# Kernel optimization log

Hardware: AMD Instinct MI355X
Metric: run time of the kernel (lower is better)

Reference implementation:

```python
import jax, jax.numpy as jnp
import numpy as np

T, B, D_POSE, H, K_CODES = 30, 1024, 135, 512, 512
EPS = 1e-5


def _bn_relu(x, g, b):
    # BatchNorm1d (training-mode batch stats, biased var) + ReLU; x: (B, C, L)
    m = x.mean(axis=(0, 2), keepdims=True)
    v = x.var(axis=(0, 2), keepdims=True)
    y = g[None, :, None] * (x - m) * jax.lax.rsqrt(v + EPS) + b[None, :, None]
    return jax.nn.relu(y)


def _conv_sk(x, w):
    # Conv1d with stride == kernel_size (non-overlapping): pure reshaped GEMM.
    # x: (B, I, L), w: (O, I, K) torch layout -> (B, O, L//K)
    Bn, I, L = x.shape
    O, _, K = w.shape
    xr = x.reshape(Bn, I, L // K, K)
    return jnp.einsum('bitk,oik->bot', xr, w)


def _convT_sk(x, w):
    # ConvTranspose1d with stride == kernel_size: x (B, I, L), w (I, O, K) torch layout
    Bn, I, L = x.shape
    _, O, K = w.shape
    return jnp.einsum('bil,iok->bolk', x, w).reshape(Bn, O, L * K)


def setup_inputs() -> dict:
    key = jax.random.key(0)
    ks = jax.random.split(key, 12)
    sc = 0.05
    inp = {
        'input_seqs': jax.random.normal(ks[0], (T, B, D_POSE), jnp.float32),
        'W_in': jax.random.normal(ks[1], (D_POSE, H), jnp.float32) * sc,
        'b_in': jnp.zeros((H,), jnp.float32),
        'w_e1': jax.random.normal(ks[2], (H, H, 5), jnp.float32) * sc,
        'g_e1': jnp.ones((H,), jnp.float32), 'b_e1': jnp.zeros((H,), jnp.float32),
        'w_e2': jax.random.normal(ks[3], (H, H, 3), jnp.float32) * sc,
        'g_e2': jnp.ones((H,), jnp.float32), 'b_e2': jnp.zeros((H,), jnp.float32),
        'w_e3': jax.random.normal(ks[4], (H, H, 2), jnp.float32) * sc,
        'g_e3': jnp.ones((H,), jnp.float32), 'b_e3': jnp.zeros((H,), jnp.float32),
        'codebook': jax.random.normal(ks[5], (K_CODES, H), jnp.float32) * sc,
        'W_q': jax.random.normal(ks[6], (H, H), jnp.float32) * sc,
        'b_q': jnp.zeros((H,), jnp.float32),
        'w_d1': jax.random.normal(ks[7], (H, H, 2), jnp.float32) * sc,
        'g_d1': jnp.ones((H,), jnp.float32), 'b_d1': jnp.zeros((H,), jnp.float32),
        'w_d2': jax.random.normal(ks[8], (H, H, 3), jnp.float32) * sc,
        'g_d2': jnp.ones((H,), jnp.float32), 'b_d2': jnp.zeros((H,), jnp.float32),
        'w_d3': jax.random.normal(ks[9], (H, H, 5), jnp.float32) * sc,
        'g_d3': jnp.ones((H,), jnp.float32), 'b_d3': jnp.zeros((H,), jnp.float32),
        'W_out': jax.random.normal(ks[10], (H, D_POSE), jnp.float32) * sc,
        'b_out': jnp.zeros((D_POSE,), jnp.float32),
    }
    return inp


def reference(input_seqs, W_in, b_in, w_e1, g_e1, b_e1, w_e2, g_e2, b_e2,
              w_e3, g_e3, b_e3, codebook, W_q, b_q,
              w_d1, g_d1, b_d1, w_d2, g_d2, b_d2, w_d3, g_d3, b_d3,
              W_out, b_out):
    commitment_cost = 0.25
    # ---- EncoderCNN ----
    h = input_seqs @ W_in + b_in              # (T, B, H)
    h = jnp.transpose(h, (1, 2, 0))           # (B, H, T)
    h = _bn_relu(_conv_sk(h, w_e1), g_e1, b_e1)   # (B, H, 6)
    h = _bn_relu(_conv_sk(h, w_e2), g_e2, b_e2)   # (B, H, 2)
    z = _bn_relu(_conv_sk(h, w_e3), g_e3, b_e3)   # (B, H, 1)

    # ---- VQ (VQ_Payam, straight-through) ----
    Bn, D, L = z.shape
    flat = jnp.transpose(z, (0, 2, 1)).reshape(-1, D)            # (B*L, D)
    dist = (jnp.sum(flat ** 2, axis=1, keepdims=True)
            + jnp.sum(codebook ** 2, axis=1)
            - 2.0 * flat @ codebook.T)                           # (B*L, K)
    idx = jnp.argmin(dist, axis=1)                               # (B*L,)
    quantized = codebook[idx]                                    # (B*L, D)
    e_latent_loss = jnp.mean((jax.lax.stop_gradient(quantized) - flat) ** 2)
    q_latent_loss = jnp.mean((quantized - jax.lax.stop_gradient(flat)) ** 2)
    vq_loss = q_latent_loss + commitment_cost * e_latent_loss
    q_st = flat + jax.lax.stop_gradient(quantized - flat)        # straight-through
    avg_probs = jnp.mean(jax.nn.one_hot(idx, K_CODES, dtype=flat.dtype), axis=0)
    perplexity = jnp.exp(-jnp.sum(avg_probs * jnp.log(avg_probs + 1e-10)))

    # ---- DecoderCNN ----
    d = q_st @ W_q + b_q                      # (B, H)
    d = d[:, :, None]                         # (B, H, 1)
    d = _bn_relu(_convT_sk(d, w_d1), g_d1, b_d1)  # (B, H, 2)
    d = _bn_relu(_convT_sk(d, w_d2), g_d2, b_d2)  # (B, H, 6)
    d = _bn_relu(_convT_sk(d, w_d3), g_d3, b_d3)  # (B, H, 30)
    recon = jnp.transpose(d, (0, 2, 1)) @ W_out + b_out           # (B, T, D_POSE)
    return recon, vq_loss, perplexity
```

## Files before the change

### kernel.cpp

```cpp
#include <hip/hip_runtime.h>
#include <math.h>


typedef __attribute__((ext_vector_type(8))) short bf16x8;
typedef __attribute__((ext_vector_type(4))) float f32x4;

__device__ __forceinline__ unsigned pk_bf16(float a, float b) {
    unsigned ua = __float_as_uint(a), ub = __float_as_uint(b);
    ua += 0x7fffu + ((ua >> 16) & 1u);
    ub += 0x7fffu + ((ub >> 16) & 1u);
    return (ua >> 16) | (ub & 0xffff0000u);
}
__device__ __forceinline__ unsigned short bfh(float x) {
    unsigned u = __float_as_uint(x);
    u += 0x7fffu + ((u >> 16) & 1u);
    return (unsigned short)(u >> 16);
}
__device__ __forceinline__ float bf2f(unsigned short h) {
    return __uint_as_float(((unsigned)h) << 16);
}

__device__ __forceinline__ void gload16(const unsigned short* g, unsigned short* l) {
    __builtin_amdgcn_global_load_lds(
        (const __attribute__((address_space(1))) unsigned int*)g,
        (__attribute__((address_space(3))) unsigned int*)l, 16, 0, 0);
}

__device__ __forceinline__ void bn4(float4& a, const float* __restrict__ s,
                                    const float* __restrict__ c) {
    float4 sv = *(const float4*)s;
    float4 cv = *(const float4*)c;
    a.x = fmaxf(fmaf(a.x, sv.x, cv.x), 0.f);
    a.y = fmaxf(fmaf(a.y, sv.y, cv.y), 0.f);
    a.z = fmaxf(fmaf(a.z, sv.z, cv.z), 0.f);
    a.w = fmaxf(fmaf(a.w, sv.w, cv.w), 0.f);
}

__device__ __forceinline__ void bn_fin_lds(const float* __restrict__ stats,
                                           const float* __restrict__ g,
                                           const float* __restrict__ b,
                                           float inv_n,
                                           float* scs, float* shs, int tid) {
    for (int c = tid; c < 512; c += 256) {
        float m = stats[c] * inv_n;
        float v = stats[512 + c] * inv_n - m * m;
        float a = (float)((double)g[c] / sqrt((double)v + 1e-5));
        scs[c] = a;
        shs[c] = b[c] - m * a;
    }
}

#define FBK  32
#define FSTR 36

__global__ __launch_bounds__(256)
void k_gemm(const float* __restrict__ Abase,
            const float* __restrict__ Wt,
            float* __restrict__ Cout,
            const float* __restrict__ bnS, const float* __restrict__ bnB,
            unsigned long long* __restrict__ amin,
            const float* __restrict__ codesq,
            int Mslice, int K, int N, int decK)
{
    __shared__ __align__(16) float As[FBK][FSTR];
    __shared__ __align__(16) float Bs[FBK][FSTR];

    const int tid = threadIdx.x;
    const int z  = blockIdx.z;
    const int n0 = blockIdx.x << 5;
    const int m0 = blockIdx.y << 5;
    const int ty = tid >> 4;
    const int tx = tid & 15;

    const int a_slice = z / decK, wk = z - a_slice * decK;
    const float* Ap = Abase + (size_t)a_slice * (size_t)Mslice * (size_t)K;
    const float* Wp = Wt    + (size_t)wk * (size_t)K * (size_t)N;

    const int sr  = tid >> 3;
    const int sc4 = (tid & 7) << 2;

    int mrow = m0 + sr;
    if (mrow > Mslice - 1) mrow = Mslice - 1;
    const float* Arow_p = Ap + (size_t)mrow * K;

    float acc[2][2];
    acc[0][0] = 0.f; acc[0][1] = 0.f; acc[1][0] = 0.f; acc[1][1] = 0.f;

    float4 pa = *(const float4*)(Arow_p + sc4);
    if (bnS != nullptr) bn4(pa, bnS + sc4, bnB + sc4);
    float4 pb = *(const float4*)(Wp + (size_t)sr * N + n0 + sc4);

    for (int k0 = 0; k0 < K; k0 += FBK) {
        __syncthreads();
        As[sc4 + 0][sr] = pa.x;
        As[sc4 + 1][sr] = pa.y;
        As[sc4 + 2][sr] = pa.z;
        As[sc4 + 3][sr] = pa.w;
        *(float4*)&Bs[sr][sc4] = pb;
        const int k0n = k0 + FBK;
        if (k0n < K) {
            pa = *(const float4*)(Arow_p + k0n + sc4);
            if (bnS != nullptr) bn4(pa, bnS + k0n + sc4, bnB + k0n + sc4);
            pb = *(const float4*)(Wp + (size_t)(k0n + sr) * N + n0 + sc4);
        }
        __syncthreads();
#pragma unroll
        for (int kk = 0; kk < FBK; ++kk) {
            float2 av = *(const float2*)&As[kk][ty << 1];
            float2 bv = *(const float2*)&Bs[kk][tx << 1];
            acc[0][0] = fmaf(av.x, bv.x, acc[0][0]);
            acc[0][1] = fmaf(av.x, bv.y, acc[0][1]);
            acc[1][0] = fmaf(av.y, bv.x, acc[1][0]);
            acc[1][1] = fmaf(av.y, bv.y, acc[1][1]);
        }
    }

    if (amin != nullptr) {
        float2 cq = *(const float2*)(codesq + n0 + (tx << 1));
#pragma unroll
        for (int i = 0; i < 2; ++i) {
            const int m = m0 + (ty << 1) + i;
            float d0 = cq.x - 2.f * acc[i][0];
            float d1 = cq.y - 2.f * acc[i][1];
            int bj = (d1 < d0) ? 1 : 0;
            float best = (d1 < d0) ? d1 : d0;
            unsigned u = __float_as_uint(best);
            u = (u & 0x80000000u) ? ~u : (u | 0x80000000u);
            unsigned long long key =
                ((unsigned long long)u << 32) | (unsigned)(n0 + (tx << 1) + bj);
#pragma unroll
            for (int off = 1; off < 16; off <<= 1) {
                unsigned long long o = __shfl_xor(key, off, 64);
                if (o < key) key = o;
            }
            if (tx == 0 && m < Mslice) atomicMin(&amin[m], key);
        }
        return;
    }

#pragma unroll
    for (int i = 0; i < 2; ++i) {
        const int m = m0 + (ty << 1) + i;
        if (m < Mslice) {
            float2 v = make_float2(acc[i][0], acc[i][1]);
            *(float2*)&Cout[((size_t)z * Mslice + m) * N + n0 + (tx << 1)] = v;
        }
    }
}

__global__ __launch_bounds__(512)
void k_out256(const unsigned short* __restrict__ Ap,
              const unsigned short* __restrict__ Bp,
              float* __restrict__ operm,
              const float* __restrict__ bias,
              int K, int N)
{
    __shared__ __align__(16) unsigned short As[2][128 * 64];
    __shared__ __align__(16) unsigned short Bs[2][256 * 64];

    const int tid  = threadIdx.x;
    const int lane = tid & 63;
    const int wave = tid >> 6;
    const int wm = (wave >> 2) << 6;
    const int wn = (wave & 3) << 6;
    const int m0 = blockIdx.y << 7;

    const int srow  = tid >> 3;
    const int selem = ((tid & 7) ^ (srow & 7)) << 3;
    const unsigned short* Asrc = Ap + (size_t)(m0 + srow) * K + selem;

    size_t boff[4];
#pragma unroll
    for (int c = 0; c < 4; ++c) {
        int brow = srow + (c << 6);
        if (brow > N - 1) brow = N - 1;
        boff[c] = (size_t)brow * K + selem;
    }

    f32x4 acc[4][4];
#pragma unroll
    for (int i = 0; i < 4; ++i)
#pragma unroll
        for (int j = 0; j < 4; ++j) acc[i][j] = (f32x4){0.f, 0.f, 0.f, 0.f};

    const int lidx = lane & 15;
    const int lq   = lane >> 4;

#pragma unroll
    for (int c = 0; c < 2; ++c)
        gload16(Asrc + (size_t)(c << 6) * K, &As[0][tid * 8 + (c << 12)]);
#pragma unroll
    for (int c = 0; c < 4; ++c)
        gload16(Bp + boff[c],                &Bs[0][tid * 8 + (c << 12)]);
    __syncthreads();

    const int nsteps = K >> 6;
    int cur = 0;
    for (int t = 0; t < nsteps; ++t) {
        if (t + 1 < nsteps) {
            const int k0n = (t + 1) << 6;
#pragma unroll
            for (int c = 0; c < 2; ++c)
                gload16(Asrc + (size_t)(c << 6) * K + k0n,
                        &As[cur ^ 1][tid * 8 + (c << 12)]);
#pragma unroll
            for (int c = 0; c < 4; ++c)
                gload16(Bp + boff[c] + k0n,
                        &Bs[cur ^ 1][tid * 8 + (c << 12)]);
        }
#pragma unroll
        for (int ks = 0; ks < 2; ++ks) {
            const int ub = (ks << 2) + lq;
            const int uo = (ub ^ (lidx & 7)) << 3;
            bf16x8 af[4], bfv[4];
#pragma unroll
            for (int t4 = 0; t4 < 4; ++t4)
                af[t4] = *(const bf16x8*)&As[cur][((wm + (t4 << 4) + lidx) << 6) + uo];
#pragma unroll
            for (int t4 = 0; t4 < 4; ++t4)
                bfv[t4] = *(const bf16x8*)&Bs[cur][((wn + (t4 << 4) + lidx) << 6) + uo];
#pragma unroll
            for (int mt = 0; mt < 4; ++mt)
#pragma unroll
                for (int nt = 0; nt < 4; ++nt)
                    acc[mt][nt] = __builtin_amdgcn_mfma_f32_16x16x32_bf16(
                        af[mt], bfv[nt], acc[mt][nt], 0, 0, 0);
        }
        __syncthreads();
        cur ^= 1;
    }

    const int rbase = lq << 2;
#pragma unroll
    for (int nt = 0; nt < 4; ++nt) {
        const int col = wn + (nt << 4) + lidx;
        if (col >= N) continue;
        const float badd = (bias != nullptr) ? bias[col] : 0.f;
#pragma unroll
        for (int mt = 0; mt < 4; ++mt) {
#pragma unroll
            for (int r = 0; r < 4; ++r) {
                float x = acc[mt][nt][r];
                const int row = m0 + wm + (mt << 4) + rbase + r;
                const int t = row >> 10, b = row & 1023;
                operm[(size_t)b * 4050 + t * 135 + col] = x + badd;
            }
        }
    }
}

__global__ __launch_bounds__(512)
void k_m256(const unsigned short* __restrict__ Abase,
            const unsigned short* __restrict__ Bt,
            unsigned short* __restrict__ Cb,
            float* __restrict__ stats,
            int Mslice, int K, int N, int decK)
{
    __shared__ __align__(16) unsigned short As[2][256 * 64];
    __shared__ __align__(16) unsigned short Bs[2][256 * 64];
    __shared__ float colsum[256], colsq[256];

    const int tid  = threadIdx.x;
    const int lane = tid & 63;
    const int wave = tid >> 6;
    const int wm = (wave >> 2) << 7;
    const int wn = (wave & 3) << 6;
    const int z  = blockIdx.z;
    const int n0 = blockIdx.x << 8;
    const int m0 = blockIdx.y << 8;

    if (stats != nullptr && tid < 256) { colsum[tid] = 0.f; colsq[tid] = 0.f; }

    const int a_slice = z / decK, wk = z - a_slice * decK;
    const unsigned short* Ap = Abase + (size_t)a_slice * (size_t)Mslice * (size_t)K;
    const unsigned short* Bp = Bt + (size_t)wk * (size_t)N * (size_t)K;

    const int srow  = tid >> 3;
    const int selem = ((tid & 7) ^ (srow & 7)) << 3;
    const unsigned short* Asrc = Ap + (size_t)(m0 + srow) * K + selem;

    size_t boff[4];
#pragma unroll
    for (int c = 0; c < 4; ++c) {
        int brow = n0 + srow + (c << 6);
        if (brow > N - 1) brow = N - 1;
        boff[c] = (size_t)brow * K + selem;
    }

    f32x4 acc[8][4];
#pragma unroll
    for (int i = 0; i < 8; ++i)
#pragma unroll
        for (int j = 0; j < 4; ++j) acc[i][j] = (f32x4){0.f, 0.f, 0.f, 0.f};

    const int lidx = lane & 15;
    const int lq   = lane >> 4;

#pragma unroll
    for (int c = 0; c < 4; ++c) {
        gload16(Asrc + (size_t)(c << 6) * K, &As[0][tid * 8 + (c << 12)]);
        gload16(Bp + boff[c],                &Bs[0][tid * 8 + (c << 12)]);
    }
    __syncthreads();

    const int nsteps = K >> 6;
    int cur = 0;
    for (int t = 0; t < nsteps; ++t) {
        if (t + 1 < nsteps) {
            const int k0n = (t + 1) << 6;
#pragma unroll
            for (int c = 0; c < 4; ++c) {
                gload16(Asrc + (size_t)(c << 6) * K + k0n,
                        &As[cur ^ 1][tid * 8 + (c << 12)]);
                gload16(Bp + boff[c] + k0n,
                        &Bs[cur ^ 1][tid * 8 + (c << 12)]);
            }
        }
#pragma unroll
        for (int ks = 0; ks < 2; ++ks) {
            const int ub = (ks << 2) + lq;
            const int uo = (ub ^ (lidx & 7)) << 3;
            bf16x8 af[8], bfv[4];
#pragma unroll
            for (int i = 0; i < 8; ++i)
                af[i] = *(const bf16x8*)&As[cur][((wm + (i << 4) + lidx) << 6) + uo];
#pragma unroll
            for (int j = 0; j < 4; ++j)
                bfv[j] = *(const bf16x8*)&Bs[cur][((wn + (j << 4) + lidx) << 6) + uo];
#pragma unroll
            for (int mt = 0; mt < 8; ++mt)
#pragma unroll
                for (int nt = 0; nt < 4; ++nt)
                    acc[mt][nt] = __builtin_amdgcn_mfma_f32_16x16x32_bf16(
                        af[mt], bfv[nt], acc[mt][nt], 0, 0, 0);
        }
        __syncthreads();
        cur ^= 1;
    }

    const int rbase = lq << 2;
#pragma unroll
    for (int nt = 0; nt < 4; ++nt) {
        const int col = n0 + wn + (nt << 4) + lidx;
        float s = 0.f, q = 0.f;
#pragma unroll
        for (int mt = 0; mt < 8; ++mt) {
#pragma unroll
            for (int r = 0; r < 4; ++r) {
                float x = acc[mt][nt][r];
                s += x; q += x * x;
                const int row = m0 + wm + (mt << 4) + rbase + r;
                Cb[((size_t)z * Mslice + row) * (size_t)N + col] = bfh(x);
            }
        }
        if (stats != nullptr) {
            s += __shfl_xor(s, 16, 64); s += __shfl_xor(s, 32, 64);
            q += __shfl_xor(q, 16, 64); q += __shfl_xor(q, 32, 64);
            if (lq == 0) {
                atomicAdd(&colsum[wn + (nt << 4) + lidx], s);
                atomicAdd(&colsq [wn + (nt << 4) + lidx], q);
            }
        }
    }
    if (stats != nullptr) {
        __syncthreads();
        if (tid < 256) {
            atomicAdd(&stats[n0 + tid],       colsum[tid]);
            atomicAdd(&stats[512 + n0 + tid], colsq[tid]);
        }
    }
}

__global__ __launch_bounds__(256)
void k_b64g(const unsigned short* __restrict__ Abase,
            const unsigned short* __restrict__ Bt,
            unsigned short* __restrict__ Cb,
            const float* __restrict__ bias,
            float* __restrict__ stats,
            int Mslice, int K, int N, int decK)
{
    __shared__ __align__(16) unsigned short As[2][64 * 64];
    __shared__ __align__(16) unsigned short Bs[2][64 * 64];
    __shared__ float colsum[64], colsq[64];

    const int tid  = threadIdx.x;
    const int lane = tid & 63;
    const int wave = tid >> 6;
    const int wm = (wave >> 1) << 5;
    const int wn = (wave & 1) << 5;
    const int z  = blockIdx.z;
    const int n0 = blockIdx.x << 6;
    const int m0 = blockIdx.y << 6;

    if (stats != nullptr && tid < 64) { colsum[tid] = 0.f; colsq[tid] = 0.f; }

    const int a_slice = z / decK, wk = z - a_slice * decK;
    const unsigned short* Ap = Abase + (size_t)a_slice * (size_t)Mslice * (size_t)K;
    const unsigned short* Bp = Bt + (size_t)wk * (size_t)N * (size_t)K;

    const int srow  = tid >> 3;
    const int selem = ((tid & 7) ^ (srow & 7)) << 3;
    const unsigned short* Asrc = Ap + (size_t)(m0 + srow) * K + selem;
    const unsigned short* Bsrc = Bp + (size_t)(n0 + srow) * K + selem;

    f32x4 acc[2][2];
#pragma unroll
    for (int i = 0; i < 2; ++i)
#pragma unroll
        for (int j = 0; j < 2; ++j) acc[i][j] = (f32x4){0.f, 0.f, 0.f, 0.f};

    const int lidx = lane & 15;
    const int lq   = lane >> 4;

#pragma unroll
    for (int c = 0; c < 2; ++c) {
        gload16(Asrc + (size_t)(c << 5) * K, &As[0][tid * 8 + (c << 11)]);
        gload16(Bsrc + (size_t)(c << 5) * K, &Bs[0][tid * 8 + (c << 11)]);
    }
    __syncthreads();

    const int nsteps = K >> 6;
    int cur = 0;
    for (int t = 0; t < nsteps; ++t) {
        if (t + 1 < nsteps) {
            const int k0n = (t + 1) << 6;
#pragma unroll
            for (int c = 0; c < 2; ++c) {
                gload16(Asrc + (size_t)(c << 5) * K + k0n,
                        &As[cur ^ 1][tid * 8 + (c << 11)]);
                gload16(Bsrc + (size_t)(c << 5) * K + k0n,
                        &Bs[cur ^ 1][tid * 8 + (c << 11)]);
            }
        }
#pragma unroll
        for (int ks = 0; ks < 2; ++ks) {
            const int ub = (ks << 2) + lq;
            const int uo = (ub ^ (lidx & 7)) << 3;
            bf16x8 af[2], bfv[2];
#pragma unroll
            for (int t2 = 0; t2 < 2; ++t2)
                af[t2] = *(const bf16x8*)&As[cur][((wm + (t2 << 4) + lidx) << 6) + uo];
#pragma unroll
            for (int t2 = 0; t2 < 2; ++t2)
                bfv[t2] = *(const bf16x8*)&Bs[cur][((wn + (t2 << 4) + lidx) << 6) + uo];
#pragma unroll
            for (int mt = 0; mt < 2; ++mt)
#pragma unroll
                for (int nt = 0; nt < 2; ++nt)
                    acc[mt][nt] = __builtin_amdgcn_mfma_f32_16x16x32_bf16(
                        af[mt], bfv[nt], acc[mt][nt], 0, 0, 0);
        }
        __syncthreads();
        cur ^= 1;
    }

    const int rbase = lq << 2;
#pragma unroll
    for (int nt = 0; nt < 2; ++nt) {
        const int col = n0 + wn + (nt << 4) + lidx;
        const float badd = (bias != nullptr) ? bias[col] : 0.f;
        float s = 0.f, q = 0.f;
#pragma unroll
        for (int mt = 0; mt < 2; ++mt) {
#pragma unroll
            for (int r = 0; r < 4; ++r) {
                float x = acc[mt][nt][r];
                s += x; q += x * x;
                const int row = m0 + wm + (mt << 4) + rbase + r;
                Cb[((size_t)z * Mslice + row) * (size_t)N + col] = bfh(x + badd);
            }
        }
        if (stats != nullptr) {
            s += __shfl_xor(s, 16, 64); s += __shfl_xor(s, 32, 64);
            q += __shfl_xor(q, 16, 64); q += __shfl_xor(q, 32, 64);
            if (lq == 0) {
                atomicAdd(&colsum[wn + (nt << 4) + lidx], s);
                atomicAdd(&colsq [wn + (nt << 4) + lidx], q);
            }
        }
    }
    if (stats != nullptr) {
        __syncthreads();
        if (tid < 64) {
            atomicAdd(&stats[n0 + tid],       colsum[tid]);
            atomicAdd(&stats[512 + n0 + tid], colsq[tid]);
        }
    }
}

__global__ __launch_bounds__(256)
void k_sp64g(const unsigned short* __restrict__ Ahg,
             const unsigned short* __restrict__ Alg,
             const unsigned short* __restrict__ Whi,
             const unsigned short* __restrict__ Wlo,
             float* __restrict__ Cout, float* __restrict__ stats,
             int Mslice, int Kp, int N, int n_terms)
{
    __shared__ __align__(16) unsigned short Ah[2][64 * 32];
    __shared__ __align__(16) unsigned short Al[2][64 * 32];
    __shared__ __align__(16) unsigned short Bh[2][64 * 32];
    __shared__ __align__(16) unsigned short Bl[2][64 * 32];
    __shared__ float colsum[64], colsq[64];

    const int tid  = threadIdx.x;
    const int lane = tid & 63;
    const int wave = tid >> 6;
    const int wm = (wave >> 1) << 5;
    const int wn = (wave & 1) << 5;
    const int z  = blockIdx.z;
    const int n0 = blockIdx.x << 6;
    const int m0 = blockIdx.y << 6;

    if (stats != nullptr && tid < 64) { colsum[tid] = 0.f; colsq[tid] = 0.f; }

    const int srow  = tid >> 2;
    const int selem = ((tid & 3) ^ (srow & 3)) << 3;

    f32x4 acc[2][2];
#pragma unroll
    for (int i = 0; i < 2; ++i)
#pragma unroll
        for (int j = 0; j < 2; ++j) acc[i][j] = (f32x4){0.f, 0.f, 0.f, 0.f};

    const int lidx = lane & 15;
    const int lq   = lane >> 4;
    const int uo   = (lq ^ (lidx & 3)) << 3;

    const int cpk = Kp >> 5;
    const int tot = n_terms * cpk;

    {
        const size_t ab = ((size_t)(z * n_terms) * Mslice + m0 + srow)
                          * (size_t)Kp + selem;
        const size_t bb = ((size_t)(n0 + srow)) * (size_t)Kp + selem;
        gload16(Ahg + ab, &Ah[0][tid * 8]);
        gload16(Alg + ab, &Al[0][tid * 8]);
        gload16(Whi + bb, &Bh[0][tid * 8]);
        gload16(Wlo + bb, &Bl[0][tid * 8]);
    }
    __syncthreads();

    int cur = 0;
    int lt = 0, lk = 32;
    if (lk >= Kp) { lk = 0; lt = 1; }
    for (int c = 0; c < tot; ++c) {
        if (c + 1 < tot) {
            const size_t ab = ((size_t)(z * n_terms + lt) * Mslice + m0 + srow)
                              * (size_t)Kp + lk + selem;
            const size_t bb = ((size_t)lt * N + n0 + srow) * (size_t)Kp + lk + selem;
            gload16(Ahg + ab, &Ah[cur ^ 1][tid * 8]);
            gload16(Alg + ab, &Al[cur ^ 1][tid * 8]);
            gload16(Whi + bb, &Bh[cur ^ 1][tid * 8]);
            gload16(Wlo + bb, &Bl[cur ^ 1][tid * 8]);
            lk += 32; if (lk >= Kp) { lk = 0; ++lt; }
        }
        bf16x8 ah[2], al[2], bh[2], bl[2];
#pragma unroll
        for (int t = 0; t < 2; ++t) {
            const int ra = ((wm + (t << 4) + lidx) << 5) + uo;
            ah[t] = *(const bf16x8*)&Ah[cur][ra];
            al[t] = *(const bf16x8*)&Al[cur][ra];
        }
#pragma unroll
        for (int t = 0; t < 2; ++t) {
            const int rb = ((wn + (t << 4) + lidx) << 5) + uo;
            bh[t] = *(const bf16x8*)&Bh[cur][rb];
            bl[t] = *(const bf16x8*)&Bl[cur][rb];
        }
#pragma unroll
        for (int mt = 0; mt < 2; ++mt)
#pragma unroll
            for (int nt = 0; nt < 2; ++nt) {
                acc[mt][nt] = __builtin_amdgcn_mfma_f32_16x16x32_bf16(
                    ah[mt], bh[nt], acc[mt][nt], 0, 0, 0);
                acc[mt][nt] = __builtin_amdgcn_mfma_f32_16x16x32_bf16(
                    al[mt], bh[nt], acc[mt][nt], 0, 0, 0);
                acc[mt][nt] = __builtin_amdgcn_mfma_f32_16x16x32_bf16(
                    ah[mt], bl[nt], acc[mt][nt], 0, 0, 0);
            }
        __syncthreads();
        cur ^= 1;
    }

    const int rbase = lq << 2;
#pragma unroll
    for (int nt = 0; nt < 2; ++nt) {
        const int col = n0 + wn + (nt << 4) + lidx;
        float s = 0.f, q = 0.f;
#pragma unroll
        for (int mt = 0; mt < 2; ++mt) {
#pragma unroll
            for (int r = 0; r < 4; ++r) {
                float x = acc[mt][nt][r];
                s += x; q += x * x;
                const int row = m0 + wm + (mt << 4) + rbase + r;
                Cout[((size_t)z * Mslice + row) * (size_t)N + col] = x;
            }
        }
        if (stats != nullptr) {
            s += __shfl_xor(s, 16, 64); s += __shfl_xor(s, 32, 64);
            q += __shfl_xor(q, 16, 64); q += __shfl_xor(q, 32, 64);
            if (lq == 0) {
                atomicAdd(&colsum[wn + (nt << 4) + lidx], s);
                atomicAdd(&colsq [wn + (nt << 4) + lidx], q);
            }
        }
    }
    if (stats != nullptr) {
        __syncthreads();
        if (tid < 64) {
            atomicAdd(&stats[n0 + tid],       colsum[tid]);
            atomicAdd(&stats[512 + n0 + tid], colsq[tid]);
        }
    }
}

__global__ __launch_bounds__(256)
void k_sp64w(const unsigned short* __restrict__ Ahg,
             const unsigned short* __restrict__ Alg,
             const unsigned short* __restrict__ Whi,
             const unsigned short* __restrict__ Wlo,
             float* __restrict__ Cout, float* __restrict__ stats,
             int Mslice, int Kp, int N, int n_terms)
{
    __shared__ __align__(16) unsigned short Ah[2][64 * 32];
    __shared__ __align__(16) unsigned short Al[2][64 * 32];
    __shared__ __align__(16) unsigned short Bh[2][128 * 32];
    __shared__ __align__(16) unsigned short Bl[2][128 * 32];
    __shared__ float colsum[128], colsq[128];

    const int tid  = threadIdx.x;
    const int lane = tid & 63;
    const int wave = tid >> 6;
    const int wm = (wave >> 1) << 5;
    const int wn = (wave & 1) << 6;
    const int z  = blockIdx.z;
    const int n0 = blockIdx.x << 7;
    const int m0 = blockIdx.y << 6;

    if (stats != nullptr && tid < 128) { colsum[tid] = 0.f; colsq[tid] = 0.f; }

    const int srow  = tid >> 2;
    const int selem = ((tid & 3) ^ (srow & 3)) << 3;

    f32x4 acc[2][4];
#pragma unroll
    for (int i = 0; i < 2; ++i)
#pragma unroll
        for (int j = 0; j < 4; ++j) acc[i][j] = (f32x4){0.f, 0.f, 0.f, 0.f};

    const int lidx = lane & 15;
    const int lq   = lane >> 4;
    const int uo   = (lq ^ (lidx & 3)) << 3;

    const int cpk = Kp >> 5;
    const int tot = n_terms * cpk;

    {
        const size_t ab = ((size_t)(z * n_terms) * Mslice + m0 + srow)
                          * (size_t)Kp + selem;
        gload16(Ahg + ab, &Ah[0][tid * 8]);
        gload16(Alg + ab, &Al[0][tid * 8]);
#pragma unroll
        for (int c = 0; c < 2; ++c) {
            const int rowB = (c << 6) + srow;
            const size_t bb = ((size_t)(n0 + rowB)) * (size_t)Kp + selem;
            gload16(Whi + bb, &Bh[0][tid * 8 + (c << 11)]);
            gload16(Wlo + bb, &Bl[0][tid * 8 + (c << 11)]);
        }
    }
    __syncthreads();

    int cur = 0;
    int lt = 0, lk = 32;
    if (lk >= Kp) { lk = 0; lt = 1; }
    for (int c = 0; c < tot; ++c) {
        if (c + 1 < tot) {
            const size_t ab = ((size_t)(z * n_terms + lt) * Mslice + m0 + srow)
                              * (size_t)Kp + lk + selem;
            gload16(Ahg + ab, &Ah[cur ^ 1][tid * 8]);
            gload16(Alg + ab, &Al[cur ^ 1][tid * 8]);
#pragma unroll
            for (int cc = 0; cc < 2; ++cc) {
                const int rowB = (cc << 6) + srow;
                const size_t bb = ((size_t)lt * N + n0 + rowB) * (size_t)Kp
                                  + lk + selem;
                gload16(Whi + bb, &Bh[cur ^ 1][tid * 8 + (cc << 11)]);
                gload16(Wlo + bb, &Bl[cur ^ 1][tid * 8 + (cc << 11)]);
            }
            lk += 32; if (lk >= Kp) { lk = 0; ++lt; }
        }
        bf16x8 ah[2], al[2], bh[4], bl[4];
#pragma unroll
        for (int t = 0; t < 2; ++t) {
            const int ra = ((wm + (t << 4) + lidx) << 5) + uo;
            ah[t] = *(const bf16x8*)&Ah[cur][ra];
            al[t] = *(const bf16x8*)&Al[cur][ra];
        }
#pragma unroll
        for (int t = 0; t < 4; ++t) {
            const int rb = ((wn + (t << 4) + lidx) << 5) + uo;
            bh[t] = *(const bf16x8*)&Bh[cur][rb];
            bl[t] = *(const bf16x8*)&Bl[cur][rb];
        }
#pragma unroll
        for (int mt = 0; mt < 2; ++mt)
#pragma unroll
            for (int nt = 0; nt < 4; ++nt) {
                acc[mt][nt] = __builtin_amdgcn_mfma_f32_16x16x32_bf16(
                    ah[mt], bh[nt], acc[mt][nt], 0, 0, 0);
                acc[mt][nt] = __builtin_amdgcn_mfma_f32_16x16x32_bf16(
                    al[mt], bh[nt], acc[mt][nt], 0, 0, 0);
                acc[mt][nt] = __builtin_amdgcn_mfma_f32_16x16x32_bf16(
                    ah[mt], bl[nt], acc[mt][nt], 0, 0, 0);
            }
        __syncthreads();
        cur ^= 1;
    }

    const int rbase = lq << 2;
#pragma unroll
    for (int nt = 0; nt < 4; ++nt) {
        const int col = n0 + wn + (nt << 4) + lidx;
        float s = 0.f, q = 0.f;
#pragma unroll
        for (int mt = 0; mt < 2; ++mt) {
#pragma unroll
            for (int r = 0; r < 4; ++r) {
                float x = acc[mt][nt][r];
                s += x; q += x * x;
                const int row = m0 + wm + (mt << 4) + rbase + r;
                Cout[((size_t)z * Mslice + row) * (size_t)N + col] = x;
            }
        }
        if (stats != nullptr) {
            s += __shfl_xor(s, 16, 64); s += __shfl_xor(s, 32, 64);
            q += __shfl_xor(q, 16, 64); q += __shfl_xor(q, 32, 64);
            if (lq == 0) {
                atomicAdd(&colsum[wn + (nt << 4) + lidx], s);
                atomicAdd(&colsq [wn + (nt << 4) + lidx], q);
            }
        }
    }
    if (stats != nullptr) {
        __syncthreads();
        if (tid < 128) {
            atomicAdd(&stats[n0 + tid],       colsum[tid]);
            atomicAdd(&stats[512 + n0 + tid], colsq[tid]);
        }
    }
}

__global__ void k_prep(float* __restrict__ zbase, unsigned long long* __restrict__ amin,
                       const float* __restrict__ codebook, float* __restrict__ codeT,
                       float* __restrict__ codesq,
                       const float* __restrict__ w_e2, unsigned short* __restrict__ whi_e2,
                       unsigned short* __restrict__ wlo_e2,
                       const float* __restrict__ w_e3, unsigned short* __restrict__ whi_e3,
                       unsigned short* __restrict__ wlo_e3,
                       const float* __restrict__ W_q,  unsigned short* __restrict__ wqb,
                       const float* __restrict__ w_d1, unsigned short* __restrict__ wd1b,
                       const float* __restrict__ w_d2, unsigned short* __restrict__ wd2b,
                       const float* __restrict__ w_d3, unsigned short* __restrict__ wd3b,
                       const float* __restrict__ W_out, unsigned short* __restrict__ woutb,
                       const float* __restrict__ in_seqs,
                       unsigned short* __restrict__ in_h, unsigned short* __restrict__ in_l,
                       const float* __restrict__ weff,
                       unsigned short* __restrict__ whi_e1,
                       unsigned short* __restrict__ wlo_e1)
{
    __shared__ float red[4];
    const int bid = blockIdx.x;
    const int tid = threadIdx.x;

    if (bid < 32) {
        int t = bid * 256 + tid;
        if (t < 6720) zbase[t] = 0.f;
        if (t < 1024) amin[t] = ~0ULL;
        return;
    }
    if (bid < 1056) {
        int idx = (bid - 32) * 256 + tid;
        int i = (idx >> 9) & 511, o = idx & 511;
        codeT[idx] = codebook[(o << 9) + i];
        return;
    }
    if (bid < 1568) {
        int c = bid - 1056;
        float s = 0.f;
        for (int i = tid; i < 512; i += 256) { float v = codebook[c * 512 + i]; s += v * v; }
        for (int off = 32; off; off >>= 1) s += __shfl_down(s, off, 64);
        if ((tid & 63) == 0) red[tid >> 6] = s;
        __syncthreads();
        if (tid == 0) codesq[c] = red[0] + red[1] + red[2] + red[3];
        return;
    }
    if (bid < 4640) {
        int idx = (bid - 1568) * 256 + tid;
        int i = idx & 511, o = (idx >> 9) & 511, k = idx >> 18;
        float v = w_e2[(((o << 9) + i) * 3) + k];
        unsigned short h = bfh(v);
        whi_e2[idx] = h; wlo_e2[idx] = bfh(v - bf2f(h));
        return;
    }
    if (bid < 6688) {
        int idx = (bid - 4640) * 256 + tid;
        int i = idx & 511, o = (idx >> 9) & 511, k = idx >> 18;
        float v = w_e3[(((o << 9) + i) * 2) + k];
        unsigned short h = bfh(v);
        whi_e3[idx] = h; wlo_e3[idx] = bfh(v - bf2f(h));
        return;
    }
    if (bid < 7712) {
        int idx = (bid - 6688) * 256 + tid;
        int i = idx & 511, o = (idx >> 9) & 511;
        wqb[idx] = bfh(W_q[((size_t)i << 9) + o]);
        return;
    }
    if (bid < 9760) {
        int idx = (bid - 7712) * 256 + tid;
        int i = idx & 511, o = (idx >> 9) & 511, k = idx >> 18;
        wd1b[idx] = bfh(w_d1[(((size_t)i << 9) + o) * 2 + k]);
        return;
    }
    if (bid < 12832) {
        int idx = (bid - 9760) * 256 + tid;
        int i = idx & 511, o = (idx >> 9) & 511, k = idx >> 18;
        wd2b[idx] = bfh(w_d2[(((size_t)i << 9) + o) * 3 + k]);
        return;
    }
    if (bid < 17952) {
        int idx = (bid - 12832) * 256 + tid;
        int i = idx & 511, o = (idx >> 9) & 511, k = idx >> 18;
        wd3b[idx] = bfh(w_d3[(((size_t)i << 9) + o) * 5 + k]);
        return;
    }
    if (bid < 18222) {
        int idx = (bid - 17952) * 256 + tid;
        if (idx >= 69120) return;
        int i = idx % 512, o = idx / 512;
        woutb[idx] = bfh(W_out[((size_t)i * 135) + o]);
        return;
    }
    if (bid < 37422) {
        int idx = (bid - 18222) * 256 + tid;
        int i = idx % 160, r = idx / 160;
        float v = (i < 135) ? in_seqs[(size_t)r * 135 + i] : 0.f;
        unsigned short h = bfh(v);
        in_h[idx] = h; in_l[idx] = bfh(v - bf2f(h));
        return;
    }
    {
        int idx = (bid - 37422) * 256 + tid;
        if (idx >= 409600) return;
        int i = idx % 160;
        int o = (idx / 160) & 511;
        int t = idx / 81920;
        float v = (i < 135) ? weff[((size_t)t * 135 + i) * 512 + o] : 0.f;
        unsigned short h = bfh(v);
        whi_e1[idx] = h;
        wlo_e1[idx] = bfh(v - bf2f(h));
    }
}

__global__ void k_repack(const float* __restrict__ w, float* __restrict__ wt,
                         int Kc, int total)
{
    int idx = blockIdx.x * 256 + threadIdx.x;
    if (idx >= total) return;
    int k = idx >> 18;
    int rem = idx & 262143;
    int i = rem >> 9, o = rem & 511;
    wt[idx] = w[(((o << 9) + i) * Kc + k)];
}

__global__ void k_bnsplit(const float* __restrict__ x,
                          const float* __restrict__ stats,
                          const float* __restrict__ g, const float* __restrict__ b,
                          float inv_n,
                          unsigned short* __restrict__ hq, unsigned short* __restrict__ lq_,
                          int total4)
{
    __shared__ __align__(16) float scs[512], shs[512];
    const int tid = threadIdx.x;
    bn_fin_lds(stats, g, b, inv_n, scs, shs, tid);
    __syncthreads();

    int idx = blockIdx.x * 256 + tid;
    if (idx >= total4) return;
    const int base = idx << 2;
    float4 f = *(const float4*)(x + base);
    const int k = base & 511;
    float4 s = *(const float4*)&scs[k];
    float4 c = *(const float4*)&shs[k];
    float y0 = fmaxf(fmaf(f.x, s.x, c.x), 0.f);
    float y1 = fmaxf(fmaf(f.y, s.y, c.y), 0.f);
    float y2 = fmaxf(fmaf(f.z, s.z, c.z), 0.f);
    float y3 = fmaxf(fmaf(f.w, s.w, c.w), 0.f);
    unsigned short h0 = bfh(y0), h1 = bfh(y1), h2 = bfh(y2), h3 = bfh(y3);
    unsigned short l0 = bfh(y0 - bf2f(h0)), l1 = bfh(y1 - bf2f(h1));
    unsigned short l2 = bfh(y2 - bf2f(h2)), l3 = bfh(y3 - bf2f(h3));
    *(uint2*)&hq[base]  = make_uint2((unsigned)h0 | ((unsigned)h1 << 16),
                                     (unsigned)h2 | ((unsigned)h3 << 16));
    *(uint2*)&lq_[base] = make_uint2((unsigned)l0 | ((unsigned)l1 << 16),
                                     (unsigned)l2 | ((unsigned)l3 << 16));
}

__global__ void k_bnapply(const unsigned short* __restrict__ x,
                          const float* __restrict__ stats,
                          const float* __restrict__ g, const float* __restrict__ b,
                          float inv_n,
                          unsigned short* __restrict__ y, int total8)
{
    __shared__ __align__(16) float scs[512], shs[512];
    const int tid = threadIdx.x;
    bn_fin_lds(stats, g, b, inv_n, scs, shs, tid);
    __syncthreads();

    int idx = blockIdx.x * 256 + tid;
    if (idx >= total8) return;
    const int base = idx << 3;
    uint4 raw = *(const uint4*)(x + base);
    const int k = base & 511;
    float4 s0 = *(const float4*)&scs[k];
    float4 c0 = *(const float4*)&shs[k];
    float4 s1 = *(const float4*)&scs[k + 4];
    float4 c1 = *(const float4*)&shs[k + 4];
    unsigned* u = (unsigned*)&raw;
    float x0 = __uint_as_float(u[0] << 16),        x1 = __uint_as_float(u[0] & 0xffff0000u);
    float x2 = __uint_as_float(u[1] << 16),        x3 = __uint_as_float(u[1] & 0xffff0000u);
    float x4 = __uint_as_float(u[2] << 16),        x5 = __uint_as_float(u[2] & 0xffff0000u);
    float x6 = __uint_as_float(u[3] << 16),        x7 = __uint_as_float(u[3] & 0xffff0000u);
    x0 = fmaxf(fmaf(x0, s0.x, c0.x), 0.f); x1 = fmaxf(fmaf(x1, s0.y, c0.y), 0.f);
    x2 = fmaxf(fmaf(x2, s0.z, c0.z), 0.f); x3 = fmaxf(fmaf(x3, s0.w, c0.w), 0.f);
    x4 = fmaxf(fmaf(x4, s1.x, c1.x), 0.f); x5 = fmaxf(fmaf(x5, s1.y, c1.y), 0.f);
    x6 = fmaxf(fmaf(x6, s1.z, c1.z), 0.f); x7 = fmaxf(fmaf(x7, s1.w, c1.w), 0.f);
    *(uint4*)&y[base] = make_uint4(pk_bf16(x0, x1), pk_bf16(x2, x3),
                                   pk_bf16(x4, x5), pk_bf16(x6, x7));
}

__global__ void k_bn_fin(const float* __restrict__ stats,
                         const float* __restrict__ g, const float* __restrict__ b,
                         float* __restrict__ sc, float* __restrict__ sh, float inv_n)
{
    int c = blockIdx.x * blockDim.x + threadIdx.x;
    if (c >= 512) return;
    float m = stats[c] * inv_n;
    float v = stats[512 + c] * inv_n - m * m;
    float a = (float)((double)g[c] / sqrt((double)v + 1e-5));
    sc[c] = a;
    sh[c] = b[c] - m * a;
}

__global__ void k_vq_gather(const unsigned long long* __restrict__ amin,
                            const float* __restrict__ codebook,
                            const float* __restrict__ e3pre,
                            const float* __restrict__ sc, const float* __restrict__ sh,
                            unsigned short* __restrict__ quant_bf,
                            float* __restrict__ loss,
                            unsigned int* __restrict__ hist)
{
    int b = blockIdx.x; int t = threadIdx.x;
    unsigned int idx = (unsigned int)(amin[b] & 0xFFFFFFFFull) & 511u;
    float part = 0.f;
    for (int i = t; i < 512; i += 256) {
        float q = codebook[(size_t)idx * 512 + i];
        quant_bf[(size_t)b * 512 + i] = bfh(q);
        float x = e3pre[(size_t)b * 512 + i];
        float f = fmaxf(fmaf(x, sc[i], sh[i]), 0.f);
        float d = q - f;
        part += d * d;
    }
    for (int off = 32; off; off >>= 1) part += __shfl_down(part, off, 64);
    __shared__ float red[4];
    if ((t & 63) == 0) red[t >> 6] = part;
    __syncthreads();
    if (t == 0) {
        atomicAdd(loss, red[0] + red[1] + red[2] + red[3]);
        atomicAdd(&hist[idx], 1u);
    }
}

__global__ void k_scalars(const unsigned int* __restrict__ hist,
                          const float* __restrict__ loss, float* __restrict__ out)
{
    int t = threadIdx.x;
    float p = (float)hist[t] * (1.0f / 1024.0f);
    float e = p * logf(p + 1e-10f);
    for (int off = 32; off; off >>= 1) e += __shfl_down(e, off, 64);
    __shared__ float red[8];
    if ((t & 63) == 0) red[t >> 6] = e;
    __syncthreads();
    if (t == 0) {
        float s = 0.f;
        for (int i = 0; i < 8; ++i) s += red[i];
        out[4147200] = 1.25f * loss[0] * (1.0f / 524288.0f);
        out[4147201] = expf(-s);
    }
}

extern "C" void kernel_launch(void* const* d_in, const int* in_sizes, int n_in,
                              void* d_out, int out_size, void* d_ws, size_t ws_size,
                              hipStream_t stream)
{
    const float* in_seqs = (const float*)d_in[0];
    const float* W_in  = (const float*)d_in[1];
    const float* w_e1  = (const float*)d_in[3];
    const float* g_e1  = (const float*)d_in[4];
    const float* be1   = (const float*)d_in[5];
    const float* w_e2  = (const float*)d_in[6];
    const float* g_e2  = (const float*)d_in[7];
    const float* be2   = (const float*)d_in[8];
    const float* w_e3  = (const float*)d_in[9];
    const float* g_e3  = (const float*)d_in[10];
    const float* be3   = (const float*)d_in[11];
    const float* codebook = (const float*)d_in[12];
    const float* W_q   = (const float*)d_in[13];
    const float* b_q   = (const float*)d_in[14];
    const float* w_d1  = (const float*)d_in[15];
    const float* g_d1  = (const float*)d_in[16];
    const float* bd1   = (const float*)d_in[17];
    const float* w_d2  = (const float*)d_in[18];
    const float* g_d2  = (const float*)d_in[19];
    const float* bd2   = (const float*)d_in[20];
    const float* w_d3  = (const float*)d_in[21];
    const float* g_d3  = (const float*)d_in[22];
    const float* bd3   = (const float*)d_in[23];
    const float* W_out = (const float*)d_in[24];
    const float* b_out = (const float*)d_in[25];
    float* out = (float*)d_out;

    float* W = (float*)d_ws;
    unsigned long long* amin = (unsigned long long*)W;
    float* stats  = W + 2048;
    float* lossp  = W + 8192;
    unsigned int* hist = (unsigned int*)(W + 8256);
    float* scsh   = W + 8768;
    float* codesq = W + 14912;
    float* wt_e1  = W + 15424;
    float* codeT  = W + 1671744;
    unsigned short* esw = (unsigned short*)(W + 1933888);
    unsigned short* whi_e1 = esw;
    unsigned short* wlo_e1 = esw + 409600;
    unsigned short* whi_e2 = esw + 819200;
    unsigned short* wlo_e2 = esw + 1605632;
    unsigned short* whi_e3 = esw + 2392064;
    unsigned short* wlo_e3 = esw + 2916352;
    unsigned short* in_h  = (unsigned short*)(W + 3654208);
    unsigned short* in_l  = in_h + 4915200;
    unsigned short* d3pre = (unsigned short*)(W + 3654208);
    float* e1f = W + 11518528;
    unsigned short* e1h = (unsigned short*)(W + 14664256);
    unsigned short* e1l = e1h + 3145728;
    float* e2f = W + 17809984;
    unsigned short* e2h = (unsigned short*)(W + 18858560);
    unsigned short* e2l = e2h + 1048576;
    unsigned short* d2pre = (unsigned short*)(W + 17809984);
    unsigned short* d2bf  = d2pre + 3145728;
    float* e3f = W + 20955712;
    unsigned short* quant_bf = (unsigned short*)(W + 21480000);
    unsigned short* d0bf     = (unsigned short*)(W + 21742144);
    unsigned short* d1pre    = (unsigned short*)(W + 22004288);
    unsigned short* d1bf     = (unsigned short*)(W + 22528640);
    unsigned short* d3bf     = (unsigned short*)(W + 23052928);
    float* weff   = W + 30917248;

    unsigned short* db    = (unsigned short*)wt_e1;
    unsigned short* wqb   = db;
    unsigned short* wd1b  = db + 262144;
    unsigned short* wd2b  = db + 786432;
    unsigned short* wd3b  = db + 1572864;
    unsigned short* woutb = db + 2883584;

    float* st_e1 = stats + 0 * 1024;
    float* st_e2 = stats + 1 * 1024;
    float* st_e3 = stats + 2 * 1024; float* sc_e3 = scsh + 2 * 1024; float* sh_e3 = sc_e3 + 512;
    float* st_d1 = stats + 3 * 1024;
    float* st_d2 = stats + 4 * 1024;
    float* st_d3 = stats + 5 * 1024;

    dim3 blk(256);

    k_repack<<<dim3(5 * 1024), blk, 0, stream>>>(w_e1, wt_e1, 5, 5 * 262144);
    k_gemm<<<dim3(16, 5, 5), blk, 0, stream>>>(W_in, wt_e1, weff,
        nullptr, nullptr, nullptr, nullptr, 135, 512, 512, 5);

    k_prep<<<dim3(39022), blk, 0, stream>>>(stats, amin,
        codebook, codeT, codesq,
        w_e2, whi_e2, wlo_e2, w_e3, whi_e3, wlo_e3,
        W_q, wqb, w_d1, wd1b, w_d2, wd2b, w_d3, wd3b, W_out, woutb,
        in_seqs, in_h, in_l, weff, whi_e1, wlo_e1);

    k_sp64w<<<dim3(4, 16, 6), blk, 0, stream>>>(in_h, in_l, whi_e1, wlo_e1,
        e1f, st_e1, 1024, 160, 512, 5);
    k_bnsplit<<<dim3(3072), blk, 0, stream>>>(e1f, st_e1, g_e1, be1,
        1.f / 6144.f, e1h, e1l, 786432);

    k_sp64g<<<dim3(8, 16, 2), blk, 0, stream>>>(e1h, e1l, whi_e2, wlo_e2,
        e2f, st_e2, 1024, 512, 512, 3);
    k_bnsplit<<<dim3(1024), blk, 0, stream>>>(e2f, st_e2, g_e2, be2,
        1.f / 2048.f, e2h, e2l, 262144);

    k_sp64g<<<dim3(8, 16, 1), blk, 0, stream>>>(e2h, e2l, whi_e3, wlo_e3,
        e3f, st_e3, 1024, 512, 512, 2);
    k_bn_fin<<<dim3(2), blk, 0, stream>>>(st_e3, g_e3, be3, sc_e3, sh_e3, 1.f / 1024.f);

    k_gemm<<<dim3(16, 32, 1), blk, 0, stream>>>(e3f, codeT, nullptr,
        sc_e3, sh_e3, amin, codesq, 1024, 512, 512, 1);
    k_vq_gather<<<dim3(1024), blk, 0, stream>>>(amin, codebook, e3f, sc_e3, sh_e3,
                                                quant_bf, lossp, hist);

    k_b64g<<<dim3(8, 16, 1), blk, 0, stream>>>(quant_bf, wqb, d0bf,
        b_q, nullptr, 1024, 512, 512, 1);

    k_b64g<<<dim3(8, 16, 2), blk, 0, stream>>>(d0bf, wd1b, d1pre,
        nullptr, st_d1, 1024, 512, 512, 2);
    k_bnapply<<<dim3(512), blk, 0, stream>>>(d1pre, st_d1, g_d1, bd1,
        1.f / 2048.f, d1bf, 131072);

    k_b64g<<<dim3(8, 16, 6), blk, 0, stream>>>(d1bf, wd2b, d2pre,
        nullptr, st_d2, 1024, 512, 512, 3);
    k_bnapply<<<dim3(1536), blk, 0, stream>>>(d2pre, st_d2, g_d2, bd2,
        1.f / 6144.f, d2bf, 393216);

    k_m256<<<dim3(2, 4, 30), dim3(512), 0, stream>>>(d2bf, wd3b, d3pre,
        st_d3, 1024, 512, 512, 5);
    k_bnapply<<<dim3(7680), blk, 0, stream>>>(d3pre, st_d3, g_d3, bd3,
        1.f / 30720.f, d3bf, 1966080);

    k_out256<<<dim3(1, 240, 1), dim3(512), 0, stream>>>(d3bf, woutb,
        out, b_out, 512, 135);

    k_scalars<<<dim3(1), dim3(512), 0, stream>>>(hist, lossp, out);
}
```

Baseline: 407.3 us.

## Fuse final decoder BatchNorm+ReLU into output GEMM operand load

Removes the separate BN-apply kernel for the last decoder layer. The output GEMM now computes BN scale/shift into LDS from the stats, then applies scale, shift and ReLU to A fragments after reading them from LDS. This saves a full pass that writes and re-reads the bf16 activation, plus one launch. In exchange, every wave that shares the same A rows redoes the per-element VALU conversion and BN math inside the MFMA loop.

```diff
diff --git a/kernel.cpp b/kernel.cpp
--- a/kernel.cpp
+++ b/kernel.cpp
@@ -34,6 +34,26 @@
     a.y = fmaxf(fmaf(a.y, sv.y, cv.y), 0.f);
     a.z = fmaxf(fmaf(a.z, sv.z, cv.z), 0.f);
     a.w = fmaxf(fmaf(a.w, sv.w, cv.w), 0.f);
+}
+
+template <int NV>
+__device__ __forceinline__ void bn_on_raw(uint4* raw, int kbase,
+                                          const float* bnS,
+                                          const float* bnB) {
+#pragma unroll
+    for (int i = 0; i < NV; ++i) {
+        unsigned* u4 = (unsigned*)&raw[i];
+#pragma unroll
+        for (int j = 0; j < 4; ++j) {
+            const int k = kbase + (i << 3) + (j << 1);
+            unsigned u = u4[j];
+            float x0 = __uint_as_float(u << 16);
+            float x1 = __uint_as_float(u & 0xffff0000u);
+            x0 = fmaxf(fmaf(x0, bnS[k],     bnB[k]),     0.f);
+            x1 = fmaxf(fmaf(x1, bnS[k + 1], bnB[k + 1]), 0.f);
+            u4[j] = pk_bf16(x0, x1);
+        }
+    }
 }
 
 __device__ __forceinline__ void bn_fin_lds(const float* __restrict__ stats,
@@ -153,10 +173,14 @@
               const unsigned short* __restrict__ Bp,
               float* __restrict__ operm,
               const float* __restrict__ bias,
+              const float* __restrict__ stats,
+              const float* __restrict__ g, const float* __restrict__ b,
+              float inv_n,
               int K, int N)
 {
     __shared__ __align__(16) unsigned short As[2][128 * 64];
     __shared__ __align__(16) unsigned short Bs[2][256 * 64];
+    __shared__ __align__(16) float scs[512], shs[512];
 
     const int tid  = threadIdx.x;
     const int lane = tid & 63;
@@ -165,6 +189,8 @@
     const int wn = (wave & 3) << 6;
     const int m0 = blockIdx.y << 7;
 
+    bn_fin_lds(stats, g, b, inv_n, scs, shs, tid);
+
     const int srow  = tid >> 3;
     const int selem = ((tid & 7) ^ (srow & 7)) << 3;
     const unsigned short* Asrc = Ap + (size_t)(m0 + srow) * K + selem;
@@ -212,10 +238,13 @@
         for (int ks = 0; ks < 2; ++ks) {
             const int ub = (ks << 2) + lq;
             const int uo = (ub ^ (lidx & 7)) << 3;
+            const int kbase = (t << 6) + (ub << 3);
             bf16x8 af[4], bfv[4];
 #pragma unroll
-            for (int t4 = 0; t4 < 4; ++t4)
+            for (int t4 = 0; t4 < 4; ++t4) {
                 af[t4] = *(const bf16x8*)&As[cur][((wm + (t4 << 4) + lidx) << 6) + uo];
+                bn_on_raw<1>((uint4*)&af[t4], kbase, scs, shs);
+            }
 #pragma unroll
             for (int t4 = 0; t4 < 4; ++t4)
                 bfv[t4] = *(const bf16x8*)&Bs[cur][((wn + (t4 << 4) + lidx) << 6) + uo];
@@ -242,8 +271,8 @@
             for (int r = 0; r < 4; ++r) {
                 float x = acc[mt][nt][r];
                 const int row = m0 + wm + (mt << 4) + rbase + r;
-                const int t = row >> 10, b = row & 1023;
-                operm[(size_t)b * 4050 + t * 135 + col] = x + badd;
+                const int t = row >> 10, bb = row & 1023;
+                operm[(size_t)bb * 4050 + t * 135 + col] = x + badd;
             }
         }
     }
@@ -1062,7 +1091,6 @@
     unsigned short* d0bf     = (unsigned short*)(W + 21742144);
     unsigned short* d1pre    = (unsigned short*)(W + 22004288);
     unsigned short* d1bf     = (unsigned short*)(W + 22528640);
-    unsigned short* d3bf     = (unsigned short*)(W + 23052928);
     float* weff   = W + 30917248;
 
     unsigned short* db    = (unsigned short*)wt_e1;
@@ -1125,11 +1153,9 @@
 
     k_m256<<<dim3(2, 4, 30), dim3(512), 0, stream>>>(d2bf, wd3b, d3pre,
         st_d3, 1024, 512, 512, 5);
-    k_bnapply<<<dim3(7680), blk, 0, stream>>>(d3pre, st_d3, g_d3, bd3,
-        1.f / 30720.f, d3bf, 1966080);
-
-    k_out256<<<dim3(1, 240, 1), dim3(512), 0, stream>>>(d3bf, woutb,
-        out, b_out, 512, 135);
+
+    k_out256<<<dim3(1, 240, 1), dim3(512), 0, stream>>>(d3pre, woutb,
+        out, b_out, st_d3, g_d3, bd3, 1.f / 30720.f, 512, 135);
 
     k_scalars<<<dim3(1), dim3(512), 0, stream>>>(hist, lossp, out);
 }
```

Result: no change. 399.5 us (-1.9%).
